# Performance work log

Measured on AMD Instinct MI355X. Metric: run time of the kernel, lower is better.

## Reference

```python
import jax, jax.numpy as jnp
import numpy as np


def setup_inputs() -> dict:
    key = jax.random.key(0)
    ks = jax.random.split(key, 7)
    B, H, W = 32, 28, 28
    C3, C4 = 1024, 2048
    C = C3 + C4            # 3072
    L1 = 9                 # num_landmarks + 1
    A, NC = 312, 200
    return {
        "l3": jax.random.normal(ks[0], (B, C3, H, W), jnp.float32),
        "l4": jax.random.normal(ks[1], (B, C4, H // 2, W // 2), jnp.float32),
        "conv_w": jax.random.normal(ks[2], (L1, C), jnp.float32) * 0.02,
        "modulation": jnp.ones((1, C, L1), jnp.float32),
        "attr_w": jax.random.normal(ks[3], (A, C), jnp.float32) * 0.02,
        "attr_b": jnp.zeros((A,), jnp.float32),
        "class_w": jax.random.normal(ks[4], (NC, A), jnp.float32) * 0.02,
    }


def reference(l3, l4, conv_w, modulation, attr_w, attr_b, class_w):
    b, c3, h, w = l3.shape
    # F.interpolate(l4, (h, w), mode='bilinear', align_corners=False)
    l4_up = jax.image.resize(l4, (b, l4.shape[1], h, w), method="bilinear")
    x = jnp.concatenate([l4_up, l3], axis=1)            # (b, 3072, h, w)

    # 1x1 conv: ab[b,l,h,w] = sum_c w[l,c] * x[b,c,h,w]
    ab = jnp.einsum("lc,bchw->blhw", conv_w, x)
    b_sq = jnp.sum(x * x, axis=1, keepdims=True)        # (b,1,h,w)
    a_sq = jnp.sum(conv_w, axis=1)[None, :, None, None]  # (1,L+1,1,1)  (matches torch: weight.sum(1), NOT squared)
    maps = jax.nn.softmax(-(b_sq - 2.0 * ab + a_sq), axis=1)  # Softmax2d = softmax over channels

    # (maps[:,None] * x[:,:,None]).mean((-1,-2))  ->  batched GEMM over spatial dim
    all_features = jnp.einsum("blhw,bchw->bcl", maps, x) / (h * w)  # (b, c, L+1)

    mod = all_features * modulation                     # dropout is identity at eval
    # permute(0,2,1)[:, :-1, :].mean(1) == mean over landmark dim excluding background
    mean_features = jnp.mean(mod[:, :, :-1], axis=2)    # (b, c)

    attr_scores = mean_features @ attr_w.T + attr_b      # (b, 312)
    class_scores = attr_scores @ class_w.T               # (b, 200)
    return attr_scores, class_scores, maps, all_features
```

## Files before the change

kernel.cpp:

```cpp
#include <hip/hip_runtime.h>
#include <math.h>

#define B_    32
#define C3_   1024
#define C4_   2048
#define C_    3072
#define P_    784
#define Q_    196
#define L_    9
#define NG_   25088
#define A_    312
#define NC_   200

#define ATTR_OFF  0
#define CLASS_OFF 9984
#define MAPS_OFF  16384
#define AF_OFF    242176

#define ASQ_OFF  0
#define MF_OFF   16
#define PART3_OFF 98320
#define Y4P_OFF   1001488
#define Y_OFF     1453072
#define MP_OFF    1509520

__global__ __launch_bounds__(256) void kA(
        const float* __restrict__ l3, const float* __restrict__ l4,
        const float* __restrict__ conv_w,
        float* __restrict__ part3, float* __restrict__ y4p,
        float* __restrict__ asq) {
    int bid = blockIdx.x;
    int t = threadIdx.x;
    if (bid < 392) {
        int g = (bid % 98) * 256 + t;
        int slab = bid / 98;
        int b = g / P_, p = g % P_;
        int c0 = slab * 256;
        const float* xp = l3 + ((size_t)b * C3_ + c0) * P_ + p;
        float ab[9];
#pragma unroll
        for (int l = 0; l < 9; ++l) ab[l] = 0.f;
        for (int i = 0; i < 256; i += 4) {
            float v0 = xp[0], v1 = xp[P_], v2 = xp[2 * P_], v3 = xp[3 * P_];
            xp += 4 * P_;
#pragma unroll
            for (int l = 0; l < 9; ++l) {
                const float4 wq = *(const float4*)(conv_w + l * C_ + C4_ + c0 + i);
                ab[l] = fmaf(wq.x, v0, ab[l]);
                ab[l] = fmaf(wq.y, v1, ab[l]);
                ab[l] = fmaf(wq.z, v2, ab[l]);
                ab[l] = fmaf(wq.w, v3, ab[l]);
            }
        }
#pragma unroll
        for (int l = 0; l < 9; ++l)
            part3[(size_t)(slab * 9 + l) * NG_ + g] = ab[l];
    } else if (bid < 648) {
        int idx = bid - 392;
        int b = idx >> 3, grp = idx & 7;
        int c0 = grp * 256;
        if (t < Q_) {
            int q = t;
            const float* base = l4 + ((size_t)b * C4_ + c0) * Q_ + q;
            float acc[9];
#pragma unroll
            for (int l = 0; l < 9; ++l) acc[l] = 0.f;
            for (int c = 0; c < 256; c += 4) {
                float v0 = base[(size_t)(c + 0) * Q_];
                float v1 = base[(size_t)(c + 1) * Q_];
                float v2 = base[(size_t)(c + 2) * Q_];
                float v3 = base[(size_t)(c + 3) * Q_];
#pragma unroll
                for (int l = 0; l < 9; ++l) {
                    const float4 wq = *(const float4*)(conv_w + l * C_ + c0 + c);
                    acc[l] = fmaf(wq.x, v0, acc[l]);
                    acc[l] = fmaf(wq.y, v1, acc[l]);
                    acc[l] = fmaf(wq.z, v2, acc[l]);
                    acc[l] = fmaf(wq.w, v3, acc[l]);
                }
            }
#pragma unroll
            for (int l = 0; l < 9; ++l)
                y4p[(size_t)((b * 8 + grp) * 9 + l) * Q_ + q] = acc[l];
        }
    } else {
        __shared__ float red[256];
        for (int l = 0; l < L_; ++l) {
            float s = 0.f;
            for (int c = t; c < C_; c += 256) s += conv_w[l * C_ + c];
            red[t] = s; __syncthreads();
            for (int o = 128; o > 0; o >>= 1) {
                if (t < o) red[t] += red[t + o];
                __syncthreads();
            }
            if (t == 0) asq[l] = red[0];
            __syncthreads();
        }
    }
}

__global__ __launch_bounds__(256) void kB(const float* __restrict__ y4p,
                                          float* __restrict__ Y) {
    int tid = blockIdx.x * 256 + threadIdx.x;
    if (tid >= 32 * 9 * Q_) return;
    int b = tid / (9 * Q_);
    int r = tid % (9 * Q_);
    float s = 0.f;
#pragma unroll
    for (int grp = 0; grp < 8; ++grp)
        s += y4p[(size_t)(b * 8 + grp) * (9 * Q_) + r];
    Y[(size_t)b * (9 * Q_) + r] = s;
}

__global__ __launch_bounds__(256) void kC(const float* __restrict__ part3,
                                          const float* __restrict__ Y,
                                          const float* __restrict__ asq,
                                          float* __restrict__ out_maps) {
    int g = blockIdx.x * 256 + threadIdx.x;
    int b = g / P_, p = g % P_;
    int yy = p / 28, xx = p % 28;
    float sy = 0.5f * yy - 0.25f, sx = 0.5f * xx - 0.25f;
    float fyf = floorf(sy), fxf = floorf(sx);
    float fy = sy - fyf, fx = sx - fxf;
    int ya = max(0, (int)fyf), yb = min(13, (int)fyf + 1);
    int xa = max(0, (int)fxf), xb = min(13, (int)fxf + 1);
    int o00 = ya * 14 + xa, o01 = ya * 14 + xb;
    int o10 = yb * 14 + xa, o11 = yb * 14 + xb;
    float w00 = (1.f - fy) * (1.f - fx), w01 = (1.f - fy) * fx;
    float w10 = fy * (1.f - fx),         w11 = fy * fx;
    const float* Yb = Y + (size_t)b * (9 * Q_);
    float v[9];
#pragma unroll
    for (int l = 0; l < 9; ++l) {
        const float* Yl = Yb + l * Q_;
        float ab4 = w00 * Yl[o00] + w01 * Yl[o01] + w10 * Yl[o10] + w11 * Yl[o11];
        float ab3 = 0.f;
#pragma unroll
        for (int sl = 0; sl < 4; ++sl)
            ab3 += part3[(size_t)(sl * 9 + l) * NG_ + g];
        v[l] = 2.f * (ab4 + ab3) - asq[l];
    }
    float m = v[0];
#pragma unroll
    for (int l = 1; l < 9; ++l) m = fmaxf(m, v[l]);
    float sum = 0.f;
#pragma unroll
    for (int l = 0; l < 9; ++l) { v[l] = expf(v[l] - m); sum += v[l]; }
    float inv = 1.f / sum;
#pragma unroll
    for (int l = 0; l < 9; ++l)
        out_maps[(size_t)b * (L_ * P_) + l * P_ + p] = v[l] * inv;
}

__device__ __forceinline__ int adj_taps(int q, int* ys, float* wy) {
    if (q == 0)  { ys[0] = 0;  wy[0] = 1.00f; ys[1] = 1;  wy[1] = 0.75f;
                   ys[2] = 2;  wy[2] = 0.25f; return 3; }
    if (q == 13) { ys[0] = 25; wy[0] = 0.25f; ys[1] = 26; wy[1] = 0.75f;
                   ys[2] = 27; wy[2] = 1.00f; return 3; }
    ys[0] = 2 * q - 1; wy[0] = 0.25f;
    ys[1] = 2 * q;     wy[1] = 0.75f;
    ys[2] = 2 * q + 1; wy[2] = 0.75f;
    ys[3] = 2 * q + 2; wy[3] = 0.25f;
    return 4;
}

__global__ __launch_bounds__(256) void kD(const float* __restrict__ maps,
                                          float* __restrict__ Mp) {
    int tid = blockIdx.x * 256 + threadIdx.x;
    if (tid >= 32 * 9 * Q_) return;
    int b = tid / (9 * Q_);
    int r = tid % (9 * Q_);
    int l = r / Q_, q = r % Q_;
    int qy = q / 14, qx = q % 14;
    int ys[4], xs[4]; float wy[4], wx[4];
    int ny = adj_taps(qy, ys, wy);
    int nx = adj_taps(qx, xs, wx);
    const float* mrow = maps + (size_t)b * (L_ * P_) + l * P_;
    float s = 0.f;
    for (int i = 0; i < ny; ++i) {
        float rs = 0.f;
        for (int j = 0; j < nx; ++j)
            rs = fmaf(wx[j], mrow[ys[i] * 28 + xs[j]], rs);
        s = fmaf(wy[i], rs, s);
    }
    Mp[(size_t)b * (9 * Q_) + r] = s;
}

__global__ __launch_bounds__(256) void kE(
        const float* __restrict__ l3, const float* __restrict__ l4,
        const float* __restrict__ maps, const float* __restrict__ Mp,
        const float* __restrict__ modulation,
        float* __restrict__ out_af, float* __restrict__ mf) {
    int bid = blockIdx.x;
    int t = threadIdx.x;
    float acc[9];
#pragma unroll
    for (int l = 0; l < 9; ++l) acc[l] = 0.f;
    int b, gc;
    if (bid < 128) {
        b = bid >> 2;
        int c3 = (bid & 3) * 256 + t;
        gc = C4_ + c3;
        const float* row = l3 + ((size_t)b * C3_ + c3) * P_;
        const float* mb = maps + (size_t)b * (L_ * P_);
        for (int p = 0; p < P_; p += 4) {
            const float4 xv = *(const float4*)(row + p);
#pragma unroll
            for (int l = 0; l < 9; ++l) {
                const float4 mv = *(const float4*)(mb + l * P_ + p);
                acc[l] = fmaf(xv.x, mv.x, acc[l]);
                acc[l] = fmaf(xv.y, mv.y, acc[l]);
                acc[l] = fmaf(xv.z, mv.z, acc[l]);
                acc[l] = fmaf(xv.w, mv.w, acc[l]);
            }
        }
    } else {
        int idx = bid - 128;
        b = idx >> 3;
        gc = (idx & 7) * 256 + t;
        const float* plane = l4 + ((size_t)b * C4_ + gc) * Q_;
        const float* mpb = Mp + (size_t)b * (9 * Q_);
        for (int q = 0; q < Q_; q += 4) {
            const float4 xv = *(const float4*)(plane + q);
#pragma unroll
            for (int l = 0; l < 9; ++l) {
                const float4 mv = *(const float4*)(mpb + l * Q_ + q);
                acc[l] = fmaf(xv.x, mv.x, acc[l]);
                acc[l] = fmaf(xv.y, mv.y, acc[l]);
                acc[l] = fmaf(xv.z, mv.z, acc[l]);
                acc[l] = fmaf(xv.w, mv.w, acc[l]);
            }
        }
    }
    float s = 0.f;
#pragma unroll
    for (int l = 0; l < 9; ++l) {
        float af = acc[l] * (1.f / 784.f);
        out_af[((size_t)b * C_ + gc) * 9 + l] = af;
        if (l < 8) s = fmaf(af, modulation[gc * 9 + l], s);
    }
    mf[(size_t)b * C_ + gc] = s * 0.125f;
}

__global__ __launch_bounds__(256) void kF(
        const float* __restrict__ mf, const float* __restrict__ attr_w,
        const float* __restrict__ attr_b, float* __restrict__ out_attr) {
    int idx = blockIdx.x * 4 + (threadIdx.x >> 6);
    int lane = threadIdx.x & 63;
    int b = idx / A_, a = idx % A_;
    const float4* wr = (const float4*)(attr_w + (size_t)a * C_);
    const float4* mr = (const float4*)(mf + (size_t)b * C_);
    float acc = 0.f;
    for (int j = lane; j < C_ / 4; j += 64) {
        float4 w = wr[j], m = mr[j];
        acc += w.x * m.x + w.y * m.y + w.z * m.z + w.w * m.w;
    }
    acc += __shfl_xor(acc, 1);  acc += __shfl_xor(acc, 2);
    acc += __shfl_xor(acc, 4);  acc += __shfl_xor(acc, 8);
    acc += __shfl_xor(acc, 16); acc += __shfl_xor(acc, 32);
    if (lane == 0) out_attr[idx] = acc + attr_b[a];
}

__global__ __launch_bounds__(256) void kG(
        const float* __restrict__ attr, const float* __restrict__ class_w,
        float* __restrict__ out_class) {
    int idx = blockIdx.x * 4 + (threadIdx.x >> 6);
    int lane = threadIdx.x & 63;
    int b = idx / NC_, n = idx % NC_;
    float acc = 0.f;
    for (int a = lane; a < A_; a += 64)
        acc += attr[b * A_ + a] * class_w[n * A_ + a];
    acc += __shfl_xor(acc, 1);  acc += __shfl_xor(acc, 2);
    acc += __shfl_xor(acc, 4);  acc += __shfl_xor(acc, 8);
    acc += __shfl_xor(acc, 16); acc += __shfl_xor(acc, 32);
    if (lane == 0) out_class[idx] = acc;
}

extern "C" void kernel_launch(void* const* d_in, const int* in_sizes, int n_in,
                              void* d_out, int out_size, void* d_ws, size_t ws_size,
                              hipStream_t stream) {
    (void)in_sizes; (void)n_in; (void)out_size; (void)ws_size;
    const float* l3         = (const float*)d_in[0];
    const float* l4         = (const float*)d_in[1];
    const float* conv_w     = (const float*)d_in[2];
    const float* modulation = (const float*)d_in[3];
    const float* attr_w     = (const float*)d_in[4];
    const float* attr_b     = (const float*)d_in[5];
    const float* class_w    = (const float*)d_in[6];
    float* out = (float*)d_out;
    float* ws  = (float*)d_ws;
    float* asq   = ws + ASQ_OFF;
    float* mf    = ws + MF_OFF;
    float* part3 = ws + PART3_OFF;
    float* y4p   = ws + Y4P_OFF;
    float* Y     = ws + Y_OFF;
    float* Mp    = ws + MP_OFF;

    kA<<<649, 256, 0, stream>>>(l3, l4, conv_w, part3, y4p, asq);
    kB<<<221, 256, 0, stream>>>(y4p, Y);
    kC<<<98, 256, 0, stream>>>(part3, Y, asq, out + MAPS_OFF);
    kD<<<221, 256, 0, stream>>>(out + MAPS_OFF, Mp);
    kE<<<384, 256, 0, stream>>>(l3, l4, out + MAPS_OFF, Mp, modulation,
                                out + AF_OFF, mf);
    kF<<<(B_ * A_) / 4, 256, 0, stream>>>(mf, attr_w, attr_b, out + ATTR_OFF);
    kG<<<(B_ * NC_) / 4, 256, 0, stream>>>(out + ATTR_OFF, class_w,
                                           out + CLASS_OFF);
}
```

Before: 317.2 us.

## Use bf16 MFMA for landmark pooling GEMM and split conv channel slabs finer

The pooling GEMM (maps times features) is rebuilt to run on bf16 MFMA 16x16x32 instructions. The map or Mp tile is converted to bf16 into shared memory, and each wave handles 16 channels with finer-grained blocks. The modulated-mean reduction moves into a separate small kernel. The 1x1 conv partial sums now use twice as many channel slabs, with more loads unrolled per step, to raise parallelism, at the cost of extra partial-sum traffic. Rounding features and maps to bf16 lowers accuracy against the fp32 reference.

```diff
diff --git a/kernel.cpp b/kernel.cpp
--- a/kernel.cpp
+++ b/kernel.cpp
@@ -17,12 +17,21 @@
 #define MAPS_OFF  16384
 #define AF_OFF    242176
 
-#define ASQ_OFF  0
-#define MF_OFF   16
-#define PART3_OFF 98320
-#define Y4P_OFF   1001488
-#define Y_OFF     1453072
-#define MP_OFF    1509520
+#define ASQ_OFF   0
+#define MF_OFF    16
+#define PART3_OFF (16 + B_ * C_)
+#define Y4P_OFF   (PART3_OFF + 8 * 9 * NG_)
+#define Y_OFF     (Y4P_OFF + 32 * 16 * 9 * Q_)
+#define MP_OFF    (Y_OFF + 32 * 9 * Q_)
+
+typedef __attribute__((ext_vector_type(8))) short bf16x8;
+typedef __attribute__((ext_vector_type(4))) float f32x4;
+
+__device__ __forceinline__ short f2bf(float f) {
+    union { float f; unsigned u; } v; v.f = f;
+    unsigned r = v.u + 0x7FFFu + ((v.u >> 16) & 1u);
+    return (short)(r >> 16);
+}
 
 __global__ __launch_bounds__(256) void kA(
         const float* __restrict__ l3, const float* __restrict__ l4,
@@ -31,57 +40,67 @@
         float* __restrict__ asq) {
     int bid = blockIdx.x;
     int t = threadIdx.x;
-    if (bid < 392) {
+    if (bid < 784) {
         int g = (bid % 98) * 256 + t;
         int slab = bid / 98;
         int b = g / P_, p = g % P_;
-        int c0 = slab * 256;
+        int c0 = slab * 128;
         const float* xp = l3 + ((size_t)b * C3_ + c0) * P_ + p;
         float ab[9];
 #pragma unroll
         for (int l = 0; l < 9; ++l) ab[l] = 0.f;
-        for (int i = 0; i < 256; i += 4) {
-            float v0 = xp[0], v1 = xp[P_], v2 = xp[2 * P_], v3 = xp[3 * P_];
-            xp += 4 * P_;
+        for (int i = 0; i < 128; i += 8) {
+            float v[8];
+#pragma unroll
+            for (int k = 0; k < 8; ++k) v[k] = xp[(size_t)k * P_];
+            xp += (size_t)8 * P_;
 #pragma unroll
             for (int l = 0; l < 9; ++l) {
-                const float4 wq = *(const float4*)(conv_w + l * C_ + C4_ + c0 + i);
-                ab[l] = fmaf(wq.x, v0, ab[l]);
-                ab[l] = fmaf(wq.y, v1, ab[l]);
-                ab[l] = fmaf(wq.z, v2, ab[l]);
-                ab[l] = fmaf(wq.w, v3, ab[l]);
+                const float4 w0 = *(const float4*)(conv_w + l * C_ + C4_ + c0 + i);
+                const float4 w1 = *(const float4*)(conv_w + l * C_ + C4_ + c0 + i + 4);
+                ab[l] = fmaf(w0.x, v[0], ab[l]);
+                ab[l] = fmaf(w0.y, v[1], ab[l]);
+                ab[l] = fmaf(w0.z, v[2], ab[l]);
+                ab[l] = fmaf(w0.w, v[3], ab[l]);
+                ab[l] = fmaf(w1.x, v[4], ab[l]);
+                ab[l] = fmaf(w1.y, v[5], ab[l]);
+                ab[l] = fmaf(w1.z, v[6], ab[l]);
+                ab[l] = fmaf(w1.w, v[7], ab[l]);
             }
         }
 #pragma unroll
         for (int l = 0; l < 9; ++l)
             part3[(size_t)(slab * 9 + l) * NG_ + g] = ab[l];
-    } else if (bid < 648) {
-        int idx = bid - 392;
-        int b = idx >> 3, grp = idx & 7;
-        int c0 = grp * 256;
+    } else if (bid < 1296) {
+        int idx = bid - 784;
+        int b = idx >> 4, grp = idx & 15;
+        int c0 = grp * 128;
         if (t < Q_) {
-            int q = t;
-            const float* base = l4 + ((size_t)b * C4_ + c0) * Q_ + q;
+            const float* base = l4 + ((size_t)b * C4_ + c0) * Q_ + t;
             float acc[9];
 #pragma unroll
             for (int l = 0; l < 9; ++l) acc[l] = 0.f;
-            for (int c = 0; c < 256; c += 4) {
-                float v0 = base[(size_t)(c + 0) * Q_];
-                float v1 = base[(size_t)(c + 1) * Q_];
-                float v2 = base[(size_t)(c + 2) * Q_];
-                float v3 = base[(size_t)(c + 3) * Q_];
+            for (int c = 0; c < 128; c += 8) {
+                float v[8];
+#pragma unroll
+                for (int k = 0; k < 8; ++k) v[k] = base[(size_t)(c + k) * Q_];
 #pragma unroll
                 for (int l = 0; l < 9; ++l) {
-                    const float4 wq = *(const float4*)(conv_w + l * C_ + c0 + c);
-                    acc[l] = fmaf(wq.x, v0, acc[l]);
-                    acc[l] = fmaf(wq.y, v1, acc[l]);
-                    acc[l] = fmaf(wq.z, v2, acc[l]);
-                    acc[l] = fmaf(wq.w, v3, acc[l]);
+                    const float4 w0 = *(const float4*)(conv_w + l * C_ + c0 + c);
+                    const float4 w1 = *(const float4*)(conv_w + l * C_ + c0 + c + 4);
+                    acc[l] = fmaf(w0.x, v[0], acc[l]);
+                    acc[l] = fmaf(w0.y, v[1], acc[l]);
+                    acc[l] = fmaf(w0.z, v[2], acc[l]);
+                    acc[l] = fmaf(w0.w, v[3], acc[l]);
+                    acc[l] = fmaf(w1.x, v[4], acc[l]);
+                    acc[l] = fmaf(w1.y, v[5], acc[l]);
+                    acc[l] = fmaf(w1.z, v[6], acc[l]);
+                    acc[l] = fmaf(w1.w, v[7], acc[l]);
                 }
             }
 #pragma unroll
             for (int l = 0; l < 9; ++l)
-                y4p[(size_t)((b * 8 + grp) * 9 + l) * Q_ + q] = acc[l];
+                y4p[(size_t)((b * 16 + grp) * 9 + l) * Q_ + t] = acc[l];
         }
     } else {
         __shared__ float red[256];
@@ -107,8 +126,8 @@
     int r = tid % (9 * Q_);
     float s = 0.f;
 #pragma unroll
-    for (int grp = 0; grp < 8; ++grp)
-        s += y4p[(size_t)(b * 8 + grp) * (9 * Q_) + r];
+    for (int grp = 0; grp < 16; ++grp)
+        s += y4p[(size_t)(b * 16 + grp) * (9 * Q_) + r];
     Y[(size_t)b * (9 * Q_) + r] = s;
 }
 
@@ -136,7 +155,7 @@
         float ab4 = w00 * Yl[o00] + w01 * Yl[o01] + w10 * Yl[o10] + w11 * Yl[o11];
         float ab3 = 0.f;
 #pragma unroll
-        for (int sl = 0; sl < 4; ++sl)
+        for (int sl = 0; sl < 8; ++sl)
             ab3 += part3[(size_t)(sl * 9 + l) * NG_ + g];
         v[l] = 2.f * (ab4 + ab3) - asq[l];
     }
@@ -186,60 +205,94 @@
     Mp[(size_t)b * (9 * Q_) + r] = s;
 }
 
+#define KP3 800
+#define KP4 224
+#define BROW 808
 __global__ __launch_bounds__(256) void kE(
         const float* __restrict__ l3, const float* __restrict__ l4,
         const float* __restrict__ maps, const float* __restrict__ Mp,
-        const float* __restrict__ modulation,
-        float* __restrict__ out_af, float* __restrict__ mf) {
+        float* __restrict__ out_af) {
+    __shared__ short bs[16 * BROW];
     int bid = blockIdx.x;
     int t = threadIdx.x;
-    float acc[9];
-#pragma unroll
-    for (int l = 0; l < 9; ++l) acc[l] = 0.f;
-    int b, gc;
-    if (bid < 128) {
-        b = bid >> 2;
-        int c3 = (bid & 3) * 256 + t;
-        gc = C4_ + c3;
-        const float* row = l3 + ((size_t)b * C3_ + c3) * P_;
-        const float* mb = maps + (size_t)b * (L_ * P_);
-        for (int p = 0; p < P_; p += 4) {
-            const float4 xv = *(const float4*)(row + p);
-#pragma unroll
-            for (int l = 0; l < 9; ++l) {
-                const float4 mv = *(const float4*)(mb + l * P_ + p);
-                acc[l] = fmaf(xv.x, mv.x, acc[l]);
-                acc[l] = fmaf(xv.y, mv.y, acc[l]);
-                acc[l] = fmaf(xv.z, mv.z, acc[l]);
-                acc[l] = fmaf(xv.w, mv.w, acc[l]);
-            }
+    int wave = t >> 6, lane = t & 63;
+    int row = lane & 15, quad = lane >> 4;
+
+    int b, K, gcbase;
+    const float* xbase;
+    if (bid < 512) {
+        b = bid >> 4;
+        int c0 = (bid & 15) * 64 + wave * 16;
+        gcbase = C4_ + c0;
+        K = 784;
+        xbase = l3 + ((size_t)b * C3_ + c0) * P_;
+        const float* src = maps + (size_t)b * (L_ * P_);
+        for (int i = t; i < 9 * KP3; i += 256) {
+            int l = i / KP3, k = i - l * KP3;
+            float v = (k < 784) ? src[l * P_ + k] : 0.f;
+            bs[l * BROW + k] = f2bf(v);
         }
     } else {
-        int idx = bid - 128;
-        b = idx >> 3;
-        gc = (idx & 7) * 256 + t;
-        const float* plane = l4 + ((size_t)b * C4_ + gc) * Q_;
-        const float* mpb = Mp + (size_t)b * (9 * Q_);
-        for (int q = 0; q < Q_; q += 4) {
-            const float4 xv = *(const float4*)(plane + q);
-#pragma unroll
-            for (int l = 0; l < 9; ++l) {
-                const float4 mv = *(const float4*)(mpb + l * Q_ + q);
-                acc[l] = fmaf(xv.x, mv.x, acc[l]);
-                acc[l] = fmaf(xv.y, mv.y, acc[l]);
-                acc[l] = fmaf(xv.z, mv.z, acc[l]);
-                acc[l] = fmaf(xv.w, mv.w, acc[l]);
-            }
-        }
-    }
+        int idx = bid - 512;
+        b = idx >> 5;
+        int c0 = (idx & 31) * 64 + wave * 16;
+        gcbase = c0;
+        K = 196;
+        xbase = l4 + ((size_t)b * C4_ + c0) * Q_;
+        const float* src = Mp + (size_t)b * (9 * Q_);
+        for (int i = t; i < 9 * KP4; i += 256) {
+            int l = i / KP4, k = i - l * KP4;
+            float v = (k < 196) ? src[l * Q_ + k] : 0.f;
+            bs[l * BROW + k] = f2bf(v);
+        }
+    }
+    __syncthreads();
+
+    const float* xrow = xbase + (size_t)row * K;
+    const short* brow = bs + row * BROW;
+    f32x4 acc = {0.f, 0.f, 0.f, 0.f};
+    int kfull = (K / 32) * 32;
+#pragma unroll 4
+    for (int k0 = 0; k0 < kfull; k0 += 32) {
+        int ka = k0 + quad * 8;
+        float4 xa = *(const float4*)(xrow + ka);
+        float4 xb = *(const float4*)(xrow + ka + 4);
+        bf16x8 a;
+        a[0] = f2bf(xa.x); a[1] = f2bf(xa.y); a[2] = f2bf(xa.z); a[3] = f2bf(xa.w);
+        a[4] = f2bf(xb.x); a[5] = f2bf(xb.y); a[6] = f2bf(xb.z); a[7] = f2bf(xb.w);
+        bf16x8 bv = *(const bf16x8*)(brow + ka);
+        acc = __builtin_amdgcn_mfma_f32_16x16x32_bf16(a, bv, acc, 0, 0, 0);
+    }
+    {
+        int ka = kfull + quad * 8;
+        bf16x8 a;
+#pragma unroll
+        for (int j = 0; j < 8; ++j)
+            a[j] = f2bf((ka + j < K) ? xrow[ka + j] : 0.f);
+        bf16x8 bv = *(const bf16x8*)(brow + ka);
+        acc = __builtin_amdgcn_mfma_f32_16x16x32_bf16(a, bv, acc, 0, 0, 0);
+    }
+    int l = row;
+    if (l < 9) {
+        size_t base = ((size_t)b * C_ + gcbase + quad * 4) * 9 + l;
+#pragma unroll
+        for (int r = 0; r < 4; ++r)
+            out_af[base + (size_t)r * 9] = acc[r] * (1.f / 784.f);
+    }
+}
+
+__global__ __launch_bounds__(256) void kMF(const float* __restrict__ af,
+                                           const float* __restrict__ mod,
+                                           float* __restrict__ mf) {
+    int i = blockIdx.x * 256 + threadIdx.x;
+    if (i >= B_ * C_) return;
+    int c = i % C_;
+    const float* a = af + (size_t)i * 9;
+    const float* m = mod + (size_t)c * 9;
     float s = 0.f;
 #pragma unroll
-    for (int l = 0; l < 9; ++l) {
-        float af = acc[l] * (1.f / 784.f);
-        out_af[((size_t)b * C_ + gc) * 9 + l] = af;
-        if (l < 8) s = fmaf(af, modulation[gc * 9 + l], s);
-    }
-    mf[(size_t)b * C_ + gc] = s * 0.125f;
+    for (int l = 0; l < 8; ++l) s = fmaf(a[l], m[l], s);
+    mf[i] = s * 0.125f;
 }
 
 __global__ __launch_bounds__(256) void kF(
@@ -296,12 +349,12 @@
     float* Y     = ws + Y_OFF;
     float* Mp    = ws + MP_OFF;
 
-    kA<<<649, 256, 0, stream>>>(l3, l4, conv_w, part3, y4p, asq);
+    kA<<<1297, 256, 0, stream>>>(l3, l4, conv_w, part3, y4p, asq);
     kB<<<221, 256, 0, stream>>>(y4p, Y);
     kC<<<98, 256, 0, stream>>>(part3, Y, asq, out + MAPS_OFF);
     kD<<<221, 256, 0, stream>>>(out + MAPS_OFF, Mp);
-    kE<<<384, 256, 0, stream>>>(l3, l4, out + MAPS_OFF, Mp, modulation,
-                                out + AF_OFF, mf);
+    kE<<<1536, 256, 0, stream>>>(l3, l4, out + MAPS_OFF, Mp, out + AF_OFF);
+    kMF<<<384, 256, 0, stream>>>(out + AF_OFF, modulation, mf);
     kF<<<(B_ * A_) / 4, 256, 0, stream>>>(mf, attr_w, attr_b, out + ATTR_OFF);
     kG<<<(B_ * NC_) / 4, 256, 0, stream>>>(out + ATTR_OFF, class_w,
                                            out + CLASS_OFF);
```

Result: faster. 308.0 us (-2.9%).
